# Kernel tuning notes

Measured on AMD Instinct MI355X. Metric: run time of the kernel, lower is better.

Reference implementation:

```python
import jax, jax.numpy as jnp
import numpy as np

B, IN_DIM, EMBED_DIM = 8192, 2048, 256
H1, H2 = 1024, 512
CODEBOOK_SIZE, N_LAYERS = 1024, 3
TEMP, COMMIT_W = 1.25, 0.25


def _l2norm(x, eps=1e-12):
    # F.normalize: x / max(||x||, eps)
    n = jnp.linalg.norm(x, axis=-1, keepdims=True)
    return x / jnp.maximum(n, eps)


def _layernorm(x, g, b, eps=1e-5):
    mu = x.mean(-1, keepdims=True)
    var = x.var(-1, keepdims=True)  # biased, matches torch LayerNorm
    return (x - mu) / jnp.sqrt(var + eps) * g + b


def _mlp(x, w1, g1, b1, w2, g2, b2, w3, normalize):
    h = _layernorm(jax.nn.silu(x @ w1), g1, b1)
    h = _layernorm(jax.nn.silu(h @ w2), g2, b2)
    h = h @ w3
    return _l2norm(h) if normalize else h


def _quantize(res, codebook, key):
    # squared euclidean distances [B, K], scaled by temperature
    dist = ((res ** 2).sum(1, keepdims=True)
            + (codebook ** 2).sum(1)[None, :]
            - 2.0 * res @ codebook.T) / TEMP
    # torch.multinomial(softmax(-dist)) == categorical with logits -dist
    ids = jax.random.categorical(key, -dist, axis=1)
    emb = codebook[ids]  # [B, D] gather
    sg = jax.lax.stop_gradient
    u = res / (jnp.linalg.norm(res, axis=-1, keepdims=True) + 1e-8)
    q = emb / (jnp.linalg.norm(emb, axis=-1, keepdims=True) + 1e-8)
    w = sg(_l2norm(u + q, eps=1e-6))
    # rotation trick: e - 2(e.w)w + 2(e.u)q  (w, u, q detached)
    emb_out = (res
               - 2.0 * (res * w).sum(-1, keepdims=True) * w
               + 2.0 * (res * sg(u)).sum(-1, keepdims=True) * sg(q))
    # QuantizeLoss (sum-reduced MSE both directions)
    loss = ((sg(res) - emb) ** 2).sum() + COMMIT_W * ((res - sg(emb)) ** 2).sum()
    return emb_out, ids, loss


def setup_inputs() -> dict:
    key = jax.random.key(0)
    ks = jax.random.split(key, 8)
    def lin(k, fan_in, fan_out):
        return (jax.random.normal(k, (fan_in, fan_out), jnp.float32)
                / np.sqrt(fan_in).astype(np.float32))
    return {
        "x": jax.random.normal(ks[0], (B, IN_DIM), jnp.float32),
        "enc_w1": lin(ks[1], IN_DIM, H1),
        "enc_g1": jnp.ones((H1,), jnp.float32),
        "enc_b1": jnp.zeros((H1,), jnp.float32),
        "enc_w2": lin(ks[2], H1, H2),
        "enc_g2": jnp.ones((H2,), jnp.float32),
        "enc_b2": jnp.zeros((H2,), jnp.float32),
        "enc_w3": lin(ks[3], H2, EMBED_DIM),
        "dec_w1": lin(ks[4], EMBED_DIM, H2),
        "dec_g1": jnp.ones((H2,), jnp.float32),
        "dec_b1": jnp.zeros((H2,), jnp.float32),
        "dec_w2": lin(ks[5], H2, H1),
        "dec_g2": jnp.ones((H1,), jnp.float32),
        "dec_b2": jnp.zeros((H1,), jnp.float32),
        "dec_w3": lin(ks[6], H1, IN_DIM),
        # nn.init.uniform_ -> U[0,1)
        "codebooks": jax.random.uniform(ks[7], (N_LAYERS, CODEBOOK_SIZE, EMBED_DIM), jnp.float32),
    }


def reference(x, enc_w1, enc_g1, enc_b1, enc_w2, enc_g2, enc_b2, enc_w3,
              dec_w1, dec_g1, dec_b1, dec_w2, dec_g2, dec_b2, dec_w3,
              codebooks):
    res = _mlp(x, enc_w1, enc_g1, enc_b1, enc_w2, enc_g2, enc_b2, enc_w3,
               normalize=False)
    keys = jax.random.split(jax.random.key(42), N_LAYERS)
    quant_loss = jnp.float32(0.0)
    embs, sem = [], []
    for i in range(N_LAYERS):  # small fixed residual depth
        e, ids, l = _quantize(res, codebooks[i], keys[i])
        quant_loss = quant_loss + l
        res = res - e
        embs.append(e)
        sem.append(ids)
    embs_arr = jnp.stack(embs, axis=-1)   # [B, D, L]
    sem_ids = jnp.stack(sem, axis=-1)     # [B, L]
    x_hat = _mlp(embs_arr.sum(-1), dec_w1, dec_g1, dec_b1, dec_w2, dec_g2,
                 dec_b2, dec_w3, normalize=True)
    recon = ((x_hat - x) ** 2).sum(-1)    # per-sample [B]
    loss = (recon + quant_loss).mean()
    embs_norm = jnp.linalg.norm(embs_arr, axis=1)  # [B, L]
    eq = (sem_ids[:, None, :] == sem_ids[None, :, :]).all(-1)  # [B, B]
    p_unique = (~jnp.triu(eq, k=1)).all(1).sum() / sem_ids.shape[0]
    return loss, recon.mean(), quant_loss, embs_norm, p_unique
```

## Files before the change

kernel.cpp:

```cpp
#include <hip/hip_runtime.h>
#include <hip/hip_bf16.h>
#include <stdint.h>
#include <math.h>

#define NB    8192
#define INDIM 2048
#define EMB   256
#define H1N   1024
#define H2N   512
#define KCB   1024
#define NLAYER 3
#define HASHN 16384

typedef _Float16 f16x8 __attribute__((ext_vector_type(8)));
typedef _Float16 f16x4 __attribute__((ext_vector_type(4)));
typedef _Float16 f16x2 __attribute__((ext_vector_type(2)));
typedef float    f32x4 __attribute__((ext_vector_type(4)));

#define LO_SCALE 1024.0f
#define LO_INV   (1.0f / 1024.0f)

#define GLD16(g, p) __builtin_amdgcn_global_load_lds( \
    (const __attribute__((address_space(1))) void*)(g), \
    (__attribute__((address_space(3))) void*)(p), 16, 0, 0)

__host__ __device__ inline void tf2x32(uint32_t k0, uint32_t k1, uint32_t x0, uint32_t x1,
                                       uint32_t& o0, uint32_t& o1)
{
  const uint32_t ks2 = 0x1BD11BDAu ^ k0 ^ k1;
  uint32_t a = x0 + k0, b = x1 + k1;
#define TF_RND(r) { a += b; b = (b << (r)) | (b >> (32 - (r))); b ^= a; }
  TF_RND(13) TF_RND(15) TF_RND(26) TF_RND(6)
  a += k1; b += ks2 + 1u;
  TF_RND(17) TF_RND(29) TF_RND(16) TF_RND(24)
  a += ks2; b += k0 + 2u;
  TF_RND(13) TF_RND(15) TF_RND(26) TF_RND(6)
  a += k0; b += k1 + 3u;
  TF_RND(17) TF_RND(29) TF_RND(16) TF_RND(24)
  a += k1; b += ks2 + 4u;
  TF_RND(13) TF_RND(15) TF_RND(26) TF_RND(6)
  a += ks2; b += k0 + 5u;
#undef TF_RND
  o0 = a; o1 = b;
}

__device__ inline float blk_reduce_sum(float v, float* sbuf)
{
  const int t = threadIdx.x;
  sbuf[t] = v; __syncthreads();
  for (int s = 128; s > 0; s >>= 1) {
    if (t < s) sbuf[t] += sbuf[t + s];
    __syncthreads();
  }
  float r = sbuf[0];
  __syncthreads();
  return r;
}

__device__ inline float wred(float v)
{
#pragma unroll
  for (int m = 32; m > 0; m >>= 1) v += __shfl_xor(v, m);
  return v;
}

template<int NS, int OUTMODE, int BM>
__global__ __launch_bounds__(BM == 256 ? 512 : 256) void mgemm(
    const _Float16* __restrict__ A0, const _Float16* __restrict__ A1,
    const _Float16* __restrict__ B0, const _Float16* __restrict__ B1,
    void* __restrict__ Cp, _Float16* __restrict__ Cs0, _Float16* __restrict__ Cs1,
    unsigned long long* __restrict__ amax, const float* __restrict__ cn2l,
    uint32_t gk0, uint32_t gk1,
    int M, int N, int K)
{
  constexpr int WAVES = (BM == 256) ? 8 : 4;
  constexpr int RPR = WAVES * 16;
  constexpr int AR = BM / RPR;
  constexpr int BR = 128 / RPR;
  constexpr int JN = (BM == 64) ? 2 : 4;
  constexpr int ASPL = BM * 64;
  constexpr int ABYTES = NS * ASPL;
  constexpr int BBYTES = NS * 8192;
  constexpr int BUF = ABYTES + BBYTES;
  __shared__ __align__(16) char sm[2 * BUF];

  const int nwg = gridDim.x * gridDim.y;
  const int bid0 = blockIdx.y * gridDim.x + blockIdx.x;
  const int cpx = nwg >> 3;
  const int swz = (bid0 & 7) * cpx + (bid0 >> 3);
  const int bx = swz % gridDim.x, by = swz / gridDim.x;

  const int tid = threadIdx.x;
  const int w = tid >> 6, l = tid & 63;
  const int wm = (BM == 64) ? 0 : (w >> 1);
  const int wn = (BM == 64) ? w : (w & 1);
  constexpr int WCOL = (BM == 64) ? 32 : 64;
  const size_t brow = (size_t)by * BM;
  const size_t bcol = (size_t)bx * 128;

  const int brow16 = w * 16 + (l >> 2);
  const int bcol16 = ((l & 3) ^ ((l >> 3) & 3)) * 8;

  const _Float16* gA0 = A0 + (brow + brow16) * (size_t)K + bcol16;
  const _Float16* gA1 = (NS >= 2) ? (A1 + (brow + brow16) * (size_t)K + bcol16) : nullptr;
  const _Float16* gB0 = B0 + (bcol + brow16) * (size_t)K + bcol16;
  const _Float16* gB1 = (NS >= 2) ? (B1 + (bcol + brow16) * (size_t)K + bcol16) : nullptr;

  auto STAGE = [&](int buf, int kk) {
    char* bA = sm + buf * BUF;
    char* bB = bA + ABYTES;
#pragma unroll
    for (int i = 0; i < AR; i++) {
      GLD16(gA0 + (size_t)(i * RPR) * K + kk, bA + i * (RPR * 64) + w * 1024);
      if constexpr (NS >= 2) GLD16(gA1 + (size_t)(i * RPR) * K + kk, bA + ASPL + i * (RPR * 64) + w * 1024);
    }
#pragma unroll
    for (int i = 0; i < BR; i++) {
      GLD16(gB0 + (size_t)(i * RPR) * K + kk, bB + i * (RPR * 64) + w * 1024);
      if constexpr (NS >= 2) GLD16(gB1 + (size_t)(i * RPR) * K + kk, bB + 8192 + i * (RPR * 64) + w * 1024);
    }
  };

  f32x4 acc0[4][JN], acc1[4][JN];
#pragma unroll
  for (int i = 0; i < 4; i++)
#pragma unroll
    for (int j = 0; j < JN; j++) {
      acc0[i][j] = (f32x4){0.f, 0.f, 0.f, 0.f};
      if constexpr (NS >= 2) acc1[i][j] = (f32x4){0.f, 0.f, 0.f, 0.f};
    }

  const int srow = l & 15;
  const int ksel = l >> 4;
  const int sel2 = (srow >> 1) & 3;
  const int fslot16 = (ksel ^ sel2) * 16;

  STAGE(0, 0);
  __syncthreads();
  int cur = 0;

  for (int k0 = 0; k0 < K; k0 += 32) {
    if (k0 + 32 < K) STAGE(cur ^ 1, k0 + 32);

    const char* smA = sm + cur * BUF;
    const char* smB = smA + ABYTES;

    f16x8 ah[4], al[4];
#pragma unroll
    for (int i = 0; i < 4; i++) {
      const int rb = (wm * 64 + i * 16 + srow) * 64 + fslot16;
      ah[i] = *(const f16x8*)(smA + rb);
      if constexpr (NS >= 2) al[i] = *(const f16x8*)(smA + ASPL + rb);
    }

#pragma unroll
    for (int j = 0; j < JN; j++) {
      const int rb = (wn * WCOL + j * 16 + srow) * 64 + fslot16;
      f16x8 bh = *(const f16x8*)(smB + rb);
      f16x8 bl{};
      if constexpr (NS >= 2) bl = *(const f16x8*)(smB + 8192 + rb);
#pragma unroll
      for (int i = 0; i < 4; i++) {
        acc0[i][j] = __builtin_amdgcn_mfma_f32_16x16x32_f16(ah[i], bh, acc0[i][j], 0, 0, 0);
        if constexpr (NS >= 2) {
          acc1[i][j] = __builtin_amdgcn_mfma_f32_16x16x32_f16(ah[i], bl, acc1[i][j], 0, 0, 0);
          acc1[i][j] = __builtin_amdgcn_mfma_f32_16x16x32_f16(al[i], bh, acc1[i][j], 0, 0, 0);
        }
      }
    }
    __syncthreads();
    cur ^= 1;
  }

  if constexpr (OUTMODE == 3) {
    const int rowb = (int)brow + wm * 64 + (l >> 4) * 4;
    const int colb = (int)bcol + wn * 64 + (l & 15);
#pragma unroll
    for (int i = 0; i < 4; i++)
#pragma unroll
      for (int r = 0; r < 4; r++) {
        const int grow = rowb + i * 16 + r;
        float bestv = -INFINITY; int bestj = 0x7fffffff;
#pragma unroll
        for (int j = 0; j < JN; j++) {
          float v = acc0[i][j][r];
          if constexpr (NS >= 2) v += acc1[i][j][r] * LO_INV;
          const int gcol = colb + j * 16;
          const uint32_t idx = (uint32_t)(grow * KCB + gcol);
          uint32_t o0, o1;
          tf2x32(gk0, gk1, 0u, idx, o0, o1);
          const uint32_t bits = o0 ^ o1;
          float f = __uint_as_float((bits >> 9) | 0x3f800000u) - 1.0f;
          float u = fmaxf(f, 1.17549435e-38f);
          float gmb = -__logf(-__logf(u));
          float val = gmb + (2.0f * v - cn2l[gcol]) / 1.25f;
          if (val > bestv || (val == bestv && gcol < bestj)) { bestv = val; bestj = gcol; }
        }
#pragma unroll
        for (int m = 1; m < 16; m <<= 1) {
          float ov = __shfl_xor(bestv, m);
          int oj = __shfl_xor(bestj, m);
          if (ov > bestv || (ov == bestv && oj < bestj)) { bestv = ov; bestj = oj; }
        }
        if ((l & 15) == 0) {
          uint32_t mb = __float_as_uint(bestv);
          mb = (mb & 0x80000000u) ? ~mb : (mb | 0x80000000u);
          unsigned long long pk = ((unsigned long long)mb << 32)
                                | (unsigned long long)(uint32_t)(~(uint32_t)bestj);
          atomicMax(amax + grow, pk);
        }
      }
  } else {
    const int crow0 = wm * 64 + (l >> 4) * 4;
    const int ccol0 = wn * WCOL + (l & 15);
#pragma unroll
    for (int i = 0; i < 4; i++)
#pragma unroll
      for (int j = 0; j < JN; j++)
#pragma unroll
        for (int r = 0; r < 4; r++) {
          float v = acc0[i][j][r];
          if constexpr (NS >= 2) v += acc1[i][j][r] * LO_INV;
          const size_t row = brow + crow0 + i * 16 + r;
          const size_t col = bcol + ccol0 + j * 16;
          const size_t o = row * N + col;
          if constexpr (OUTMODE == 0) {
            ((float*)Cp)[o] = v;
          } else if constexpr (OUTMODE == 1) {
            ((_Float16*)Cp)[o] = (_Float16)v;
          } else {
            ((float*)Cp)[o] = v;
            _Float16 h = (_Float16)v;
            Cs0[o] = h;
            Cs1[o] = (_Float16)((v - (float)h) * LO_SCALE);
          }
        }
  }
}

struct PrepArgs {
  const float* w[6];
  _Float16* t0[6];
  _Float16* t1[6];
  int K[6], N[6];
  int off[7];
  const float* x;
  _Float16* xh; _Float16* xl;
  const float* cb;
  _Float16* cbh; _Float16* cbl;
  float* cn2;
  unsigned long long* amax;
  int cvtBlocks;
};

__global__ __launch_bounds__(256) void prep_all(PrepArgs P)
{
  __shared__ float shf[33 * 32];
  const int b = blockIdx.x, t = threadIdx.x;

  if (b < P.off[6]) {
    int j = 0;
    while (b >= P.off[j + 1]) j++;
    const int lb = b - P.off[j];
    const int K = P.K[j], N = P.N[j];
    const int nbx = N / 32;
    const int nb = (lb % nbx) * 32, kb = (lb / nbx) * 32;
    const float* Wsrc = P.w[j];
    _Float16* T0 = P.t0[j];
    _Float16* T1 = P.t1[j];
    const int tx = t & 31, ty = t >> 5;
#pragma unroll
    for (int i = 0; i < 32; i += 8)
      shf[(ty + i) * 33 + tx] = Wsrc[(size_t)(kb + ty + i) * N + nb + tx];
    __syncthreads();
#pragma unroll
    for (int i = 0; i < 32; i += 8) {
      float v = shf[tx * 33 + ty + i];
      size_t o = (size_t)(nb + ty + i) * K + kb + tx;
      _Float16 h = (_Float16)v;
      T0[o] = h;
      if (T1) T1[o] = (_Float16)((v - (float)h) * LO_SCALE);
    }
  } else if (b < P.off[6] + P.cvtBlocks) {
    const int i = ((b - P.off[6]) * 256 + t) * 8;
    float4 va = *(const float4*)(P.x + i);
    float4 vb = *(const float4*)(P.x + i + 4);
    float f[8] = {va.x, va.y, va.z, va.w, vb.x, vb.y, vb.z, vb.w};
    f16x8 hv, lv;
#pragma unroll
    for (int e = 0; e < 8; e++) {
      _Float16 h = (_Float16)f[e];
      hv[e] = h;
      lv[e] = (_Float16)((f[e] - (float)h) * LO_SCALE);
    }
    *(f16x8*)(P.xh + i) = hv;
    *(f16x8*)(P.xl + i) = lv;
  } else if (b < P.off[6] + P.cvtBlocks + NLAYER * KCB) {
    const int r = b - P.off[6] - P.cvtBlocks;
    const size_t o = (size_t)r * EMB + t;
    const float v = P.cb[o];
    _Float16 h = (_Float16)v;
    P.cbh[o] = h;
    P.cbl[o] = (_Float16)((v - (float)h) * LO_SCALE);
    float s = blk_reduce_sum(v * v, shf);
    if (t == 0) P.cn2[r] = s;
  } else {
    const int i = (b - P.off[6] - P.cvtBlocks - NLAYER * KCB) * 256 + t;
    if (i < NB) P.amax[i] = 0ull;
  }
}

template<int NCOL, int NS, int IN16>
__global__ __launch_bounds__(256) void silu_ln(const void* __restrict__ inp,
                                               const float* __restrict__ g,
                                               const float* __restrict__ bta,
                                               _Float16* __restrict__ o0,
                                               _Float16* __restrict__ o1)
{
  constexpr int PT = NCOL / 256;
  __shared__ float sb[256];
  const int b = blockIdx.x, t = threadIdx.x;
  const int c0 = t * PT;
  float v[PT];
  if constexpr (IN16) {
    const _Float16* row = (const _Float16*)inp + (size_t)b * NCOL;
    if constexpr (PT == 4) {
      f16x4 xv = *(const f16x4*)(row + c0);
#pragma unroll
      for (int i = 0; i < 4; i++) v[i] = (float)xv[i];
    } else {
      f16x2 xv = *(const f16x2*)(row + c0);
      v[0] = (float)xv[0]; v[1] = (float)xv[1];
    }
  } else {
    const float* row = (const float*)inp + (size_t)b * NCOL;
    if constexpr (PT == 4) {
      float4 xv = *(const float4*)(row + c0);
      v[0] = xv.x; v[1] = xv.y; v[2] = xv.z; v[3] = xv.w;
    } else {
      float2 xv = *(const float2*)(row + c0);
      v[0] = xv.x; v[1] = xv.y;
    }
  }
  float s = 0.f;
#pragma unroll
  for (int i = 0; i < PT; i++) {
    float sv = v[i] / (1.f + expf(-v[i]));
    v[i] = sv; s += sv;
  }
  s = blk_reduce_sum(s, sb);
  const float mu = s / (float)NCOL;
  float q = 0.f;
#pragma unroll
  for (int i = 0; i < PT; i++) { float d = v[i] - mu; q += d * d; }
  q = blk_reduce_sum(q, sb);
  const float inv = 1.f / sqrtf(q / (float)NCOL + 1e-5f);

  float gv[PT], bv[PT];
  if constexpr (PT == 4) {
    float4 g4 = *(const float4*)(g + c0);
    float4 b4 = *(const float4*)(bta + c0);
    gv[0]=g4.x; gv[1]=g4.y; gv[2]=g4.z; gv[3]=g4.w;
    bv[0]=b4.x; bv[1]=b4.y; bv[2]=b4.z; bv[3]=b4.w;
  } else {
    float2 g2 = *(const float2*)(g + c0);
    float2 b2 = *(const float2*)(bta + c0);
    gv[0]=g2.x; gv[1]=g2.y; bv[0]=b2.x; bv[1]=b2.y;
  }
  const size_t ob = (size_t)b * NCOL + c0;
  if constexpr (PT == 4) {
    f16x4 h4, l4;
#pragma unroll
    for (int i = 0; i < 4; i++) {
      float y = (v[i] - mu) * inv * gv[i] + bv[i];
      _Float16 h = (_Float16)y;
      h4[i] = h;
      if constexpr (NS >= 2) l4[i] = (_Float16)((y - (float)h) * LO_SCALE);
    }
    *(f16x4*)(o0 + ob) = h4;
    if constexpr (NS >= 2) *(f16x4*)(o1 + ob) = l4;
  } else {
    f16x2 h2, l2;
#pragma unroll
    for (int i = 0; i < 2; i++) {
      float y = (v[i] - mu) * inv * gv[i] + bv[i];
      _Float16 h = (_Float16)y;
      h2[i] = h;
      if constexpr (NS >= 2) l2[i] = (_Float16)((y - (float)h) * LO_SCALE);
    }
    *(f16x2*)(o0 + ob) = h2;
    if constexpr (NS >= 2) *(f16x2*)(o1 + ob) = l2;
  }
}

__global__ __launch_bounds__(256) void sample_update(
    unsigned long long* __restrict__ amax,
    const float* __restrict__ cbf,
    float* __restrict__ res, float* __restrict__ esum,
    float* __restrict__ qrow, float* __restrict__ outEn,
    _Float16* __restrict__ r0, _Float16* __restrict__ r1,
    _Float16* __restrict__ esumb, int* __restrict__ ids,
    uint32_t* __restrict__ packed, int layer)
{
  const int t = threadIdx.x, w = t >> 6, l = t & 63;
  const int b = blockIdx.x * 4 + w;

  const unsigned long long pk = amax[b];
  const int id = (int)(~(uint32_t)(pk & 0xFFFFFFFFull));
  if (l == 0) {
    ids[b * NLAYER + layer] = id;
    if (layer == NLAYER - 1)
      packed[b] = (uint32_t)ids[b * NLAYER] | ((uint32_t)ids[b * NLAYER + 1] << 10)
                | ((uint32_t)id << 20);
    else
      amax[b] = 0ull;
  }

  const size_t base = (size_t)b * EMB + l * 4;
  float4 r4 = *(const float4*)(res + base);
  float4 e4 = *(const float4*)(cbf + (size_t)id * EMB + l * 4);
  float r_[4] = {r4.x, r4.y, r4.z, r4.w};
  float e_[4] = {e4.x, e4.y, e4.z, e4.w};

  float a0 = 0.f, a1 = 0.f;
#pragma unroll
  for (int i = 0; i < 4; i++) { a0 += r_[i] * r_[i]; a1 += e_[i] * e_[i]; }
  const float rn2 = wred(a0), en2 = wred(a1);
  const float rn = sqrtf(rn2), en = sqrtf(en2);
  float u_[4], q_[4], s_[4];
  float a2 = 0.f;
#pragma unroll
  for (int i = 0; i < 4; i++) {
    u_[i] = r_[i] / (rn + 1e-8f);
    q_[i] = e_[i] / (en + 1e-8f);
    s_[i] = u_[i] + q_[i];
    a2 += s_[i] * s_[i];
  }
  const float sn2 = wred(a2);
  const float wn_ = 1.f / fmaxf(sqrtf(sn2), 1e-6f);
  float a3 = 0.f, a4 = 0.f;
#pragma unroll
  for (int i = 0; i < 4; i++) {
    a3 += r_[i] * s_[i] * wn_;
    a4 += r_[i] * u_[i];
  }
  const float rw = wred(a3), ru = wred(a4);
  float eo[4];
  float a5 = 0.f, a6 = 0.f;
#pragma unroll
  for (int i = 0; i < 4; i++) {
    eo[i] = r_[i] - 2.f * rw * (s_[i] * wn_) + 2.f * ru * q_[i];
    a5 += eo[i] * eo[i];
    float dq = r_[i] - e_[i];
    a6 += dq * dq;
  }
  const float eo2 = wred(a5), ql = wred(a6);

  if (l == 0) {
    outEn[b * NLAYER + layer] = sqrtf(eo2);
    if (layer == 0) qrow[b] = 1.25f * ql; else qrow[b] += 1.25f * ql;
  }

  float nr[4];
#pragma unroll
  for (int i = 0; i < 4; i++) nr[i] = r_[i] - eo[i];
  if (layer != NLAYER - 1) {
    *(float4*)(res + base) = make_float4(nr[0], nr[1], nr[2], nr[3]);
    f16x4 h4, l4;
#pragma unroll
    for (int i = 0; i < 4; i++) {
      _Float16 h = (_Float16)nr[i];
      h4[i] = h;
      l4[i] = (_Float16)((nr[i] - (float)h) * LO_SCALE);
    }
    *(f16x4*)(r0 + base) = h4;
    *(f16x4*)(r1 + base) = l4;
  }
  float ns[4];
#pragma unroll
  for (int i = 0; i < 4; i++) ns[i] = (layer == 0) ? eo[i] : esum[base + i] + eo[i];
  if (layer != NLAYER - 1) {
    *(float4*)(esum + base) = make_float4(ns[0], ns[1], ns[2], ns[3]);
  } else {
    f16x4 h4;
#pragma unroll
    for (int i = 0; i < 4; i++) h4[i] = (_Float16)ns[i];
    *(f16x4*)(esumb + base) = h4;
  }
}

__global__ __launch_bounds__(256) void l2norm_recon(const _Float16* __restrict__ y,
                                                    const float* __restrict__ x,
                                                    float* __restrict__ recon)
{
  const int t = threadIdx.x, w = t >> 6, l = t & 63;
  const int b = blockIdx.x * 4 + w;
  const _Float16* yr = y + (size_t)b * INDIM;
  const float* xr = x + (size_t)b * INDIM;

  float vy[32], xf[32];
  float ss = 0.f;
#pragma unroll
  for (int i = 0; i < 4; i++) {
    const int c = l * 8 + i * 512;
    f16x8 v8 = *(const f16x8*)(yr + c);
    float4 xa = *(const float4*)(xr + c);
    float4 xb = *(const float4*)(xr + c + 4);
    xf[i*8+0]=xa.x; xf[i*8+1]=xa.y; xf[i*8+2]=xa.z; xf[i*8+3]=xa.w;
    xf[i*8+4]=xb.x; xf[i*8+5]=xb.y; xf[i*8+6]=xb.z; xf[i*8+7]=xb.w;
#pragma unroll
    for (int j = 0; j < 8; j++) { vy[i*8+j] = (float)v8[j]; ss += vy[i*8+j] * vy[i*8+j]; }
  }
  ss = wred(ss);
  const float inv = 1.f / fmaxf(sqrtf(ss), 1e-12f);
  float acc = 0.f;
#pragma unroll
  for (int i = 0; i < 32; i++) {
    float d = vy[i] * inv - xf[i];
    acc += d * d;
  }
  acc = wred(acc);
  if (l == 0) recon[b] = acc;
}

__global__ __launch_bounds__(256) void finalize2(const float* __restrict__ recon,
                                                 const float* __restrict__ qrow,
                                                 const uint32_t* __restrict__ packed,
                                                 float* __restrict__ out)
{
  __shared__ uint32_t tab[HASHN];
  __shared__ double sd[256];
  __shared__ int    si[256];
  const int t = threadIdx.x;
  for (int i = t; i < HASHN; i += 256) tab[i] = 0xFFFFFFFFu;
  __syncthreads();

  int my = 0;
  double aR = 0.0, aQ = 0.0;
  for (int i = t; i < NB; i += 256) {
    aR += (double)recon[i];
    aQ += (double)qrow[i];
    const uint32_t v = packed[i];
    uint32_t h = (v * 2654435761u) & (HASHN - 1);
    while (true) {
      uint32_t old = atomicCAS(&tab[h], 0xFFFFFFFFu, v);
      if (old == 0xFFFFFFFFu) { my++; break; }
      if (old == v) break;
      h = (h + 1) & (HASHN - 1);
    }
  }
  sd[t] = aR; si[t] = my; __syncthreads();
  for (int s = 128; s > 0; s >>= 1) {
    if (t < s) { sd[t] += sd[t + s]; si[t] += si[t + s]; }
    __syncthreads();
  }
  const double sumR = sd[0]; const int dcnt = si[0]; __syncthreads();
  sd[t] = aQ; __syncthreads();
  for (int s = 128; s > 0; s >>= 1) { if (t < s) sd[t] += sd[t + s]; __syncthreads(); }
  const double sumQ = sd[0];
  if (t == 0) {
    const float rm = (float)(sumR / (double)NB);
    const float ql = (float)sumQ;
    out[0] = rm + ql;
    out[1] = rm;
    out[2] = ql;
    out[3 + NB * NLAYER] = (float)dcnt / (float)NB;
  }
}

extern "C" void kernel_launch(void* const* d_in, const int* in_sizes, int n_in,
                              void* d_out, int out_size, void* d_ws, size_t ws_size,
                              hipStream_t stream)
{
  const float* x      = (const float*)d_in[0];
  const float* enc_w1 = (const float*)d_in[1];
  const float* enc_g1 = (const float*)d_in[2];
  const float* enc_b1 = (const float*)d_in[3];
  const float* enc_w2 = (const float*)d_in[4];
  const float* enc_g2 = (const float*)d_in[5];
  const float* enc_b2 = (const float*)d_in[6];
  const float* enc_w3 = (const float*)d_in[7];
  const float* dec_w1 = (const float*)d_in[8];
  const float* dec_g1 = (const float*)d_in[9];
  const float* dec_b1 = (const float*)d_in[10];
  const float* dec_w2 = (const float*)d_in[11];
  const float* dec_g2 = (const float*)d_in[12];
  const float* dec_b2 = (const float*)d_in[13];
  const float* dec_w3 = (const float*)d_in[14];
  const float* codebooks = (const float*)d_in[15];
  float* out = (float*)d_out;

  char* W = (char*)d_ws;
  _Float16* xh   = (_Float16*)(W + 0);
  _Float16* h1n0 = (_Float16*)(W + 0);
  _Float16* h1n1 = (_Float16*)(W + 16777216);
  _Float16* h2n0 = (_Float16*)(W + 0);
  _Float16* h2n1 = (_Float16*)(W + 8388608);
  _Float16* res0 = (_Float16*)(W + 16777216);
  _Float16* res1 = (_Float16*)(W + 20971520);
  _Float16* d1n  = (_Float16*)(W + 0);
  _Float16* d2n  = (_Float16*)(W + 25165824);
  _Float16* xl    = (_Float16*)(W + 33554432);
  float*    h2    = (float*)  (W + 33554432);
  _Float16* d1h   = (_Float16*)(W + 33554432);
  float*    res32 = (float*)  (W + 50331648);
  float*    esum32= (float*)  (W + 58720256);
  float*    h1 = (float*)    (W + 67108864);
  _Float16* d2h = (_Float16*)(W + 67108864);
  _Float16* yb = (_Float16*) (W + 67108864);
  _Float16* w1t0 = (_Float16*)(W + 100663296);
  _Float16* w1t1 = (_Float16*)(W + 104857600);
  _Float16* w2t0 = (_Float16*)(W + 109051904);
  _Float16* w2t1 = (_Float16*)(W + 110100480);
  _Float16* w3t0 = (_Float16*)(W + 111149056);
  _Float16* w3t1 = (_Float16*)(W + 111411200);
  _Float16* dw1t = (_Float16*)(W + 111673344);
  _Float16* dw2t = (_Float16*)(W + 111935488);
  _Float16* dw3t = (_Float16*)(W + 112984064);
  _Float16* cbh  = (_Float16*)(W + 117178368);
  _Float16* cbl  = (_Float16*)(W + 118751232);
  _Float16* esumb= (_Float16*)(W + 120324096);
  float* cn2   = (float*)(W + 124518400);
  float* recon = (float*)(W + 124534784);
  float* qrow  = (float*)(W + 124567552);
  int*   ids   = (int*)  (W + 124600320);
  uint32_t* packed = (uint32_t*)(W + 124698624);
  unsigned long long* amax = (unsigned long long*)(W + 124850176);

  uint32_t key0[NLAYER], key1[NLAYER];
  for (int l = 0; l < NLAYER; l++) tf2x32(0u, 42u, 0u, (uint32_t)l, key0[l], key1[l]);

  dim3 blk(256), blk512(512);
  PrepArgs P;
  P.w[0] = enc_w1; P.t0[0] = w1t0; P.t1[0] = w1t1; P.K[0] = INDIM; P.N[0] = H1N;
  P.w[1] = enc_w2; P.t0[1] = w2t0; P.t1[1] = w2t1; P.K[1] = H1N;   P.N[1] = H2N;
  P.w[2] = enc_w3; P.t0[2] = w3t0; P.t1[2] = w3t1; P.K[2] = H2N;   P.N[2] = EMB;
  P.w[3] = dec_w1; P.t0[3] = dw1t; P.t1[3] = nullptr; P.K[3] = EMB; P.N[3] = H2N;
  P.w[4] = dec_w2; P.t0[4] = dw2t; P.t1[4] = nullptr; P.K[4] = H2N; P.N[4] = H1N;
  P.w[5] = dec_w3; P.t0[5] = dw3t; P.t1[5] = nullptr; P.K[5] = H1N; P.N[5] = INDIM;
  P.off[0] = 0;
  for (int j = 0; j < 6; j++) P.off[j + 1] = P.off[j] + (P.N[j] / 32) * (P.K[j] / 32);
  P.x = x; P.xh = xh; P.xl = xl;
  P.cb = codebooks; P.cbh = cbh; P.cbl = cbl; P.cn2 = cn2;
  P.amax = amax;
  P.cvtBlocks = (NB * INDIM) / 2048;
  const int prepGrid = P.off[6] + P.cvtBlocks + NLAYER * KCB + NB / 256;
  prep_all<<<prepGrid, blk, 0, stream>>>(P);

  mgemm<2,0,256><<<dim3(H1N/128, NB/256), blk512, 0, stream>>>(xh, xl, w1t0, w1t1,
      h1, nullptr, nullptr, nullptr, nullptr, 0u, 0u, NB, H1N, INDIM);
  silu_ln<H1N,2,0><<<NB, blk, 0, stream>>>(h1, enc_g1, enc_b1, h1n0, h1n1);
  mgemm<2,0,128><<<dim3(H2N/128, NB/128), blk, 0, stream>>>(h1n0, h1n1, w2t0, w2t1,
      h2, nullptr, nullptr, nullptr, nullptr, 0u, 0u, NB, H2N, H1N);
  silu_ln<H2N,2,0><<<NB, blk, 0, stream>>>(h2, enc_g2, enc_b2, h2n0, h2n1);
  mgemm<2,2,64><<<dim3(EMB/128, NB/64), blk, 0, stream>>>(h2n0, h2n1, w3t0, w3t1,
      res32, res0, res1, nullptr, nullptr, 0u, 0u, NB, EMB, H2N);

  for (int l = 0; l < NLAYER; l++) {
    const float* cbfl = codebooks + (size_t)l * KCB * EMB;
    const size_t co = (size_t)l * KCB * EMB;
    mgemm<2,3,256><<<dim3(KCB/128, NB/256), blk512, 0, stream>>>(res0, res1,
        cbh + co, cbl + co, nullptr, nullptr, nullptr,
        amax, cn2 + l * KCB, key0[l], key1[l], NB, KCB, EMB);
    sample_update<<<NB/4, blk, 0, stream>>>(amax, cbfl,
        res32, esum32, qrow, out + 3, res0, res1, esumb, ids, packed, l);
  }

  mgemm<1,1,128><<<dim3(H2N/128, NB/128), blk, 0, stream>>>(esumb, nullptr, dw1t, nullptr,
      d1h, nullptr, nullptr, nullptr, nullptr, 0u, 0u, NB, H2N, EMB);
  silu_ln<H2N,1,1><<<NB, blk, 0, stream>>>(d1h, dec_g1, dec_b1, d1n, nullptr);
  mgemm<1,1,128><<<dim3(H1N/128, NB/128), blk, 0, stream>>>(d1n, nullptr, dw2t, nullptr,
      d2h, nullptr, nullptr, nullptr, nullptr, 0u, 0u, NB, H1N, H2N);
  silu_ln<H1N,1,1><<<NB, blk, 0, stream>>>(d2h, dec_g2, dec_b2, d2n, nullptr);
  mgemm<1,1,256><<<dim3(INDIM/128, NB/256), blk512, 0, stream>>>(d2n, nullptr, dw3t, nullptr,
      yb, nullptr, nullptr, nullptr, nullptr, 0u, 0u, NB, INDIM, H1N);
  l2norm_recon<<<NB/4, blk, 0, stream>>>(yb, x, recon);

  finalize2<<<1, blk, 0, stream>>>(recon, qrow, packed, out);
}
```

Before: 549.2 us.

## Triple-buffer LDS staging with explicit vmcnt waits for BM=256 GEMM tiles

For the 256-row GEMM variant, the shared-memory ring grows from two to three k-stages and loads are issued two stages ahead. Each step waits with an explicit s_waitcnt vmcnt on the outstanding global-to-LDS loads, then a raw s_barrier, in place of __syncthreads. The aim is to hide global load latency behind more MFMA work and avoid full drains. The cost is 50% more LDS per block, which may lower occupancy, and the hand-counted vmcnt values depend on the exact number of loads per stage being right.

```diff
diff --git a/kernel.cpp b/kernel.cpp
--- a/kernel.cpp
+++ b/kernel.cpp
@@ -23,6 +23,10 @@
 #define GLD16(g, p) __builtin_amdgcn_global_load_lds( \
     (const __attribute__((address_space(1))) void*)(g), \
     (__attribute__((address_space(3))) void*)(p), 16, 0, 0)
+
+template<int N> __device__ inline void waitv() {
+  asm volatile("s_waitcnt vmcnt(%0)" :: "i"(N) : "memory");
+}
 
 __host__ __device__ inline void tf2x32(uint32_t k0, uint32_t k1, uint32_t x0, uint32_t x1,
                                        uint32_t& o0, uint32_t& o1)
@@ -77,12 +81,14 @@
   constexpr int RPR = WAVES * 16;
   constexpr int AR = BM / RPR;
   constexpr int BR = 128 / RPR;
+  constexpr int LPS = NS * (AR + BR);
   constexpr int JN = (BM == 64) ? 2 : 4;
   constexpr int ASPL = BM * 64;
   constexpr int ABYTES = NS * ASPL;
   constexpr int BBYTES = NS * 8192;
   constexpr int BUF = ABYTES + BBYTES;
-  __shared__ __align__(16) char sm[2 * BUF];
+  constexpr int NBUF = (BM == 256) ? 3 : 2;
+  __shared__ __align__(16) char sm[NBUF * BUF];
 
   const int nwg = gridDim.x * gridDim.y;
   const int bid0 = blockIdx.y * gridDim.x + blockIdx.x;
@@ -135,16 +141,9 @@
   const int sel2 = (srow >> 1) & 3;
   const int fslot16 = (ksel ^ sel2) * 16;
 
-  STAGE(0, 0);
-  __syncthreads();
-  int cur = 0;
-
-  for (int k0 = 0; k0 < K; k0 += 32) {
-    if (k0 + 32 < K) STAGE(cur ^ 1, k0 + 32);
-
-    const char* smA = sm + cur * BUF;
+  auto COMPUTE = [&](int buf) {
+    const char* smA = sm + buf * BUF;
     const char* smB = smA + ABYTES;
-
     f16x8 ah[4], al[4];
 #pragma unroll
     for (int i = 0; i < 4; i++) {
@@ -152,7 +151,6 @@
       ah[i] = *(const f16x8*)(smA + rb);
       if constexpr (NS >= 2) al[i] = *(const f16x8*)(smA + ASPL + rb);
     }
-
 #pragma unroll
     for (int j = 0; j < JN; j++) {
       const int rb = (wn * WCOL + j * 16 + srow) * 64 + fslot16;
@@ -168,8 +166,36 @@
         }
       }
     }
+  };
+
+  if constexpr (BM == 256) {
+    const int kst = K / 32;
+    STAGE(0, 0);
+    STAGE(1, 32);
+    STAGE(2, 64);
+    for (int i = 0; i < kst; ++i) {
+      if (i + 2 < kst)      waitv<2 * LPS>();
+      else if (i + 1 < kst) waitv<LPS>();
+      else                  waitv<0>();
+      __builtin_amdgcn_s_barrier();
+      __builtin_amdgcn_sched_barrier(0);
+      COMPUTE(i % 3);
+      __builtin_amdgcn_sched_barrier(0);
+      __builtin_amdgcn_s_barrier();
+      if (i + 3 < kst) STAGE(i % 3, (i + 3) * 32);
+      __builtin_amdgcn_sched_barrier(0);
+    }
+    asm volatile("s_waitcnt lgkmcnt(0)" ::: "memory");
+  } else {
+    STAGE(0, 0);
     __syncthreads();
-    cur ^= 1;
+    int cur = 0;
+    for (int k0 = 0; k0 < K; k0 += 32) {
+      if (k0 + 32 < K) STAGE(cur ^ 1, k0 + 32);
+      COMPUTE(cur);
+      __syncthreads();
+      cur ^= 1;
+    }
   }
 
   if constexpr (OUTMODE == 3) {
```

Measured after the change: 555.4 us. Within noise of the previous version (+1.1%).
